# Performance work log

Hardware: AMD Instinct MI355X
Metric: run time of the kernel (lower is better)

Reference implementation:

```python
import jax, jax.numpy as jnp
from jax import lax
import numpy as np

# dims
V, D, T = 30000, 300, 24          # vocab, glove dim, seq len
H = 256                            # tweet_out_size == z_dim
NT, NU = 6000, 4000                # tweet nodes, user nodes
N = NT + NU
F, Z = 512, 256                    # user_feat_size, z_dim
E = 80000
B = 2000                           # batch_size (source tweets)
H1, H2, HEADS = 64, 100, 8
NEG = 0.2                          # GATConv default negative_slope


def setup_inputs() -> dict:
    k = jax.random.split(jax.random.key(0), 32)
    r = lambda i, shape, s=0.05: (s * jax.random.normal(k[i], shape)).astype(jnp.float32)
    return {
        "user_text": jax.random.randint(k[0], (B, T), 0, V),
        "user_feats": jax.random.normal(k[1], (NU, F), jnp.float32),
        "graph_node_features": jax.random.randint(k[2], (NT, T), 0, V),
        "graph_edge_index": jax.random.randint(k[3], (2, E), 0, N),
        "tweet_emb": r(4, (V, D), 0.1),
        "w_ih0": r(5, (3 * H, D)), "w_hh0": r(6, (3 * H, H)),
        "b_ih0": r(7, (3 * H,)), "b_hh0": r(8, (3 * H,)),
        "w_ih1": r(9, (3 * H, H)), "w_hh1": r(10, (3 * H, H)),
        "b_ih1": r(11, (3 * H,)), "b_hh1": r(12, (3 * H,)),
        "h0": r(13, (2, NT, H), 1.0),
        "w_mu": r(14, (Z, F)), "b_mu": r(15, (Z,)),
        "w_lv": r(16, (Z, F)), "b_lv": r(17, (Z,)),
        "w_dec": r(18, (F, Z)), "b_dec": r(19, (F,)),
        "vae_eps": r(20, (NU, Z), 1.0),
        "w1": r(21, (H, HEADS * H1)), "a_src1": r(22, (HEADS, H1)),
        "a_dst1": r(23, (HEADS, H1)), "b1": r(24, (HEADS * H1,)),
        "w2": r(25, (HEADS * H1, H2)), "a_src2": r(26, (1, H2)),
        "a_dst2": r(27, (1, H2)), "b2": r(28, (H2,)),
    }


def _gru_layer(x_seq, h0, w_ih, w_hh, b_ih, b_hh):
    # x_seq: [T, B, in]; torch nn.GRU gate math
    def step(h, x):
        gi = x @ w_ih.T + b_ih
        gh = h @ w_hh.T + b_hh
        i_r, i_z, i_n = jnp.split(gi, 3, axis=-1)
        h_r, h_z, h_n = jnp.split(gh, 3, axis=-1)
        r = jax.nn.sigmoid(i_r + h_r)
        z = jax.nn.sigmoid(i_z + h_z)
        n = jnp.tanh(i_n + r * h_n)
        hn = (1.0 - z) * n + z * h
        return hn, hn
    h_last, out = lax.scan(step, h0, x_seq)
    return out, h_last


def _gat(x, src, dst, w, a_src, a_dst, bias, heads, out_ch, concat):
    # PyG GATConv (eval mode, self-loops already appended)
    n = x.shape[0]
    xp = (x @ w).reshape(n, heads, out_ch)          # [N, H, C]
    as_n = (xp * a_src).sum(-1)                     # [N, H]
    ad_n = (xp * a_dst).sum(-1)
    e = jax.nn.leaky_relu(as_n[src] + ad_n[dst], NEG)          # [E, H]
    emax = jax.ops.segment_max(e, dst, num_segments=n)         # edge-softmax over dst
    ee = jnp.exp(e - emax[dst])
    denom = jax.ops.segment_sum(ee, dst, num_segments=n)
    alpha = ee / denom[dst]
    out = jax.ops.segment_sum(xp[src] * alpha[:, :, None], dst, num_segments=n)
    out = out.reshape(n, heads * out_ch) if concat else out.mean(axis=1)
    return out + bias


def reference(user_text, user_feats, graph_node_features, graph_edge_index,
              tweet_emb, w_ih0, w_hh0, b_ih0, b_hh0, w_ih1, w_hh1, b_ih1, b_hh1,
              h0, w_mu, b_mu, w_lv, b_lv, w_dec, b_dec, vae_eps,
              w1, a_src1, a_dst1, b1, w2, a_src2, a_dst2, b2):
    # --- VAE user embedding ---
    mu = user_feats @ w_mu.T + b_mu
    logvar = user_feats @ w_lv.T + b_lv
    z = mu + jnp.exp(0.5 * logvar) * vae_eps        # reparameterized latent
    rec = z @ w_dec.T + b_dec
    kl_loss = (-0.5 * (1.0 + logvar - mu**2 - jnp.exp(logvar)).sum(-1)).mean()
    rec_loss = ((rec - user_feats) ** 2).mean()
    # --- tweet encoder: embedding lookup + 2-layer GRU ---
    xe = tweet_emb[graph_node_features].transpose(1, 0, 2)     # [T, NT, D]
    out0, _ = _gru_layer(xe, h0[0], w_ih0, w_hh0, b_ih0, b_hh0)
    _, hn = _gru_layer(out0, h0[1], w_ih1, w_hh1, b_ih1, b_hh1)  # [NT, H]
    # --- assemble node features: source tweets, users, other tweets ---
    x_in = jnp.concatenate([hn[:B], z, hn[B:]], axis=0)        # [N, H]
    loops = jnp.arange(x_in.shape[0])
    src = jnp.concatenate([graph_edge_index[0], loops])
    dst = jnp.concatenate([graph_edge_index[1], loops])
    x1 = _gat(x_in, src, dst, w1, a_src1, a_dst1, b1, HEADS, H1, True)
    x2 = _gat(x1, src, dst, w2, a_src2, a_dst2, b2, 1, H2, False)
    return x2, kl_loss, rec_loss
```

## Files before the change

kernel.cpp:

```cpp
#include <hip/hip_runtime.h>

#define V_ 30000
#define D_ 300
#define DP_ 320
#define T_ 24
#define H_ 256
#define NT_ 6000
#define NU_ 4000
#define N_ 10000
#define F_ 512
#define Z_ 256
#define E_ 80000
#define B_ 2000
#define H1_ 64
#define H2_ 100
#define HEADS_ 8
#define E2_ (E_ + N_)

typedef __bf16 bf16_t;
typedef bf16_t bf16x8 __attribute__((ext_vector_type(8)));
typedef float  f32x4  __attribute__((ext_vector_type(4)));

__device__ __forceinline__ void gll16(const bf16_t* g, bf16_t* l)
{
    __builtin_amdgcn_global_load_lds(
        (const __attribute__((address_space(1))) void*)g,
        (__attribute__((address_space(3))) void*)l, 16, 0, 0);
}

struct GCfg {
    const bf16_t* A; const bf16_t* B; const float* bias;
    float* Cf; bf16_t* Cb; int M, N, K, ldc;
    const int* gtok; int t0;
};

template<bool OUTBF>
__global__ __launch_bounds__(256) void mfma_gemm(GCfg g0, GCfg g1)
{
    const GCfg g = blockIdx.z ? g1 : g0;
    __shared__ __align__(16) bf16_t SMEM[16384];
    const int tid  = (int)threadIdx.x;
    const int wave = tid >> 6, lane = tid & 63;
    const int quad = lane >> 4, l16 = lane & 15;
    const int mq = (wave & 1) * 64, nq = (wave >> 1) * 64;

    int bx = (int)blockIdx.x, by = (int)blockIdx.y;
    {
        int gx = (int)gridDim.x, total = gx * (int)gridDim.y;
        if ((total & 7) == 0) {
            int L = by * gx + bx;
            int F = (L & 7) * (total >> 3) + (L >> 3);
            bx = F % gx;
            by = F / gx;
        }
    }
    const int mbase = by * 128, nbase = bx * 128;
    const int M = g.M, N = g.N, K = g.K, ldc = g.ldc;

    const bf16_t* agp[2];
    const bf16_t* bgp[2];
#pragma unroll
    for (int j = 0; j < 2; j++) {
        int i = wave * 128 + j * 64 + lane;
        int c = i >> 7, row = i & 127;
        int r = mbase + row; if (r >= M) r = M - 1;
        int src = g.gtok ? g.gtok[(r % NT_) * T_ + g.t0 + (r / NT_)] : r;
        agp[j] = g.A + (size_t)src * K + c * 8;
        int rb = nbase + row; if (rb >= N) rb = N - 1;
        bgp[j] = g.B + (size_t)rb * K + c * 8;
    }

    f32x4 acc[4][4];
#pragma unroll
    for (int mi = 0; mi < 4; mi++)
#pragma unroll
        for (int ni = 0; ni < 4; ni++) acc[mi][ni] = (f32x4){0.f, 0.f, 0.f, 0.f};

    auto stage = [&](int b, int k0) {
        bf16_t* ab = SMEM + b * 4096 + wave * 1024;
        bf16_t* bb = SMEM + 8192 + b * 4096 + wave * 1024;
        gll16(agp[0] + k0, ab);
        gll16(agp[1] + k0, ab + 512);
        gll16(bgp[0] + k0, bb);
        gll16(bgp[1] + k0, bb + 512);
    };

    const int niter = K >> 5;
    stage(0, 0);
    for (int ks = 0; ks < niter; ks++) {
        __syncthreads();
        if (ks + 1 < niter) stage((ks + 1) & 1, (ks + 1) * 32);
        const bf16_t* Ab = SMEM + (ks & 1) * 4096;
        const bf16_t* Bb = SMEM + 8192 + (ks & 1) * 4096;
        bf16x8 afr[4], bfr[4];
#pragma unroll
        for (int mi = 0; mi < 4; mi++)
            afr[mi] = *(const bf16x8*)(Ab + (size_t)(quad * 128 + mq + mi * 16 + l16) * 8);
#pragma unroll
        for (int ni = 0; ni < 4; ni++)
            bfr[ni] = *(const bf16x8*)(Bb + (size_t)(quad * 128 + nq + ni * 16 + l16) * 8);
#pragma unroll
        for (int mi = 0; mi < 4; mi++)
#pragma unroll
            for (int ni = 0; ni < 4; ni++)
                acc[mi][ni] = __builtin_amdgcn_mfma_f32_16x16x32_bf16(
                    afr[mi], bfr[ni], acc[mi][ni], 0, 0, 0);
    }

    if (OUTBF) {
        __syncthreads();
#pragma unroll
        for (int ni = 0; ni < 4; ni++) {
            int colc = nq + ni * 16 + l16;
            float bv = g.bias ? g.bias[nbase + colc] : 0.f;
            int cc = colc >> 3, off = colc & 7;
#pragma unroll
            for (int mi = 0; mi < 4; mi++)
#pragma unroll
                for (int r = 0; r < 4; r++) {
                    int row = mq + mi * 16 + quad * 4 + r;
                    int sw = (row ^ (row >> 3)) & 7;
                    SMEM[row * 128 + ((cc ^ sw) << 3) + off] =
                        (bf16_t)(acc[mi][ni][r] + bv);
                }
        }
        __syncthreads();
        {
            int row = tid >> 1, seg = tid & 1;
            int sw = (row ^ (row >> 3)) & 7;
            int growr = mbase + row;
            if (growr < M) {
#pragma unroll
                for (int q = 0; q < 8; q++) {
                    int cc = seg * 8 + q;
                    bf16x8 v = *(const bf16x8*)(SMEM + row * 128 + ((cc ^ sw) << 3));
                    *(bf16x8*)(g.Cb + (size_t)growr * ldc + nbase + cc * 8) = v;
                }
            }
        }
    } else {
#pragma unroll
        for (int ni = 0; ni < 4; ni++) {
            int col = nbase + nq + ni * 16 + l16;
            if (col >= N) continue;
            float bv = g.bias ? g.bias[col] : 0.f;
#pragma unroll
            for (int mi = 0; mi < 4; mi++)
#pragma unroll
                for (int r = 0; r < 4; r++) {
                    int row = mbase + mq + mi * 16 + quad * 4 + r;
                    if (row >= M) continue;
                    g.Cf[(size_t)row * ldc + col] = acc[mi][ni][r] + bv;
                }
        }
    }
}

struct MegaLay {
    const bf16_t* vocGi;
    const int*    gnf;
    const bf16_t* whh0;
    const bf16_t* wih1;
    const bf16_t* whh1;
    const float *bhh0, *bih1, *bhh1;
    const bf16_t* h0in;
    const bf16_t* h1in;
    bf16_t*       xinout;
};

__device__ __forceinline__ float rcp_(float x)
{
    float r;
    asm("v_rcp_f32 %0, %1" : "=v"(r) : "v"(x));
    return r;
}
__device__ __forceinline__ float sigm_(float x)
{
    return rcp_(1.f + __expf(-x));
}
__device__ __forceinline__ float tanh_(float x)
{
    x = fminf(fmaxf(x, -15.f), 15.f);
    float t = __expf(2.f * x);
    return 1.f - 2.f * rcp_(t + 1.f);
}

#define HSW(Hb, row, byte) ((char*)(Hb) + ((((row) * 512) + (byte)) ^ (((row) & 7) << 4)))

__global__ __launch_bounds__(512, 1) void gru_mega(MegaLay L)
{
    __shared__ __align__(16) bf16_t H0L[8192];
    __shared__ __align__(16) bf16_t H1L[8192];
    __shared__ int TOK[768];
    const int tid  = (int)threadIdx.x;
    const int wv   = tid >> 6, lane = tid & 63;
    const int quad = lane >> 4, l16 = lane & 15;
    const int row0 = (int)blockIdx.x * 32;

    for (int i = tid; i < 768; i += 512) {
        int gi = row0 * T_ + i; if (gi >= NT_ * T_) gi = NT_ * T_ - 1;
        TOK[i] = L.gnf[gi];
    }
#pragma unroll
    for (int i = 0; i < 2; i++) {
        int idx  = i * 512 + tid;
        int rowl = idx >> 5, seg = idx & 31;
        int grow = row0 + rowl; if (grow >= NT_) grow = NT_ - 1;
        *(bf16x8*)HSW(H0L, rowl, seg * 16) =
            *(const bf16x8*)(L.h0in + (size_t)grow * H_ + seg * 8);
        *(bf16x8*)HSW(H1L, rowl, seg * 16) =
            *(const bf16x8*)(L.h1in + (size_t)grow * H_ + seg * 8);
    }

    float bh0[3][2], brz1[2][2], bni1[2], bnh1[2];
#pragma unroll
    for (int jj = 0; jj < 2; jj++) {
        int col = wv * 32 + jj * 16 + l16;
        bh0[0][jj] = L.bhh0[col];
        bh0[1][jj] = L.bhh0[256 + col];
        bh0[2][jj] = L.bhh0[512 + col];
        brz1[0][jj] = L.bih1[col] + L.bhh1[col];
        brz1[1][jj] = L.bih1[256 + col] + L.bhh1[256 + col];
        bni1[jj]    = L.bih1[512 + col];
        bnh1[jj]    = L.bhh1[512 + col];
    }

    auto run_gemm = [&](auto&& loadA, const bf16_t* W,
                        f32x4 (&arz)[2][2][2], f32x4 (&an)[2][2]) {
#pragma unroll 2
        for (int ks = 0; ks < 8; ks++) {
            bf16x8 bfr[3][2];
#pragma unroll
            for (int g = 0; g < 3; g++)
#pragma unroll
                for (int jj = 0; jj < 2; jj++)
                    bfr[g][jj] = *(const bf16x8*)(W +
                        (((size_t)(g * 16 + wv * 2 + jj) * 8 + ks) << 9) + lane * 8);
            bf16x8 afr[2];
            loadA(afr, ks);
#pragma unroll
            for (int m = 0; m < 2; m++)
#pragma unroll
                for (int jj = 0; jj < 2; jj++) {
                    arz[m][0][jj] = __builtin_amdgcn_mfma_f32_16x16x32_bf16(
                        afr[m], bfr[0][jj], arz[m][0][jj], 0, 0, 0);
                    arz[m][1][jj] = __builtin_amdgcn_mfma_f32_16x16x32_bf16(
                        afr[m], bfr[1][jj], arz[m][1][jj], 0, 0, 0);
                    an[m][jj] = __builtin_amdgcn_mfma_f32_16x16x32_bf16(
                        afr[m], bfr[2][jj], an[m][jj], 0, 0, 0);
                }
        }
    };

    __syncthreads();

    for (int t = 0; t < T_; t++) {
        f32x4 arz[2][2][2], an_i[2][2], an_h[2][2], gin[2][2];

#pragma unroll
        for (int m = 0; m < 2; m++)
#pragma unroll
            for (int r2 = 0; r2 < 4; r2++) {
                int rowl = m * 16 + quad * 4 + r2;
                const bf16_t* gp = L.vocGi +
                    (size_t)TOK[rowl * T_ + t] * (3 * H_);
#pragma unroll
                for (int jj = 0; jj < 2; jj++) {
                    int col = wv * 32 + jj * 16 + l16;
                    arz[m][0][jj][r2] = (float)gp[col];
                    arz[m][1][jj][r2] = (float)gp[256 + col];
                    gin[m][jj][r2]    = (float)gp[512 + col];
                }
            }
#pragma unroll
        for (int m = 0; m < 2; m++)
#pragma unroll
            for (int jj = 0; jj < 2; jj++)
                an_h[m][jj] = (f32x4){0.f, 0.f, 0.f, 0.f};

        run_gemm([&](bf16x8* afr, int ks) {
#pragma unroll
            for (int m = 0; m < 2; m++)
                afr[m] = *(const bf16x8*)HSW(H0L, m * 16 + l16,
                                             ks * 64 + quad * 16);
        }, L.whh0, arz, an_h);
        __syncthreads();

#pragma unroll
        for (int m = 0; m < 2; m++)
#pragma unroll
            for (int jj = 0; jj < 2; jj++) {
                int col = wv * 32 + jj * 16 + l16;
#pragma unroll
                for (int r = 0; r < 4; r++) {
                    int rowl = m * 16 + quad * 4 + r;
                    float hold = (float)*(const bf16_t*)HSW(H0L, rowl, col * 2);
                    float rg = sigm_(arz[m][0][jj][r] + bh0[0][jj]);
                    float zg = sigm_(arz[m][1][jj][r] + bh0[1][jj]);
                    float ng = tanh_(gin[m][jj][r] +
                                     rg * (an_h[m][jj][r] + bh0[2][jj]));
                    *(bf16_t*)HSW(H0L, rowl, col * 2) =
                        (bf16_t)((1.f - zg) * ng + zg * hold);
                }
            }
        __syncthreads();

#pragma unroll
        for (int m = 0; m < 2; m++)
#pragma unroll
            for (int jj = 0; jj < 2; jj++) {
                arz[m][0][jj] = (f32x4){0.f, 0.f, 0.f, 0.f};
                arz[m][1][jj] = (f32x4){0.f, 0.f, 0.f, 0.f};
                an_i[m][jj]   = (f32x4){0.f, 0.f, 0.f, 0.f};
                an_h[m][jj]   = (f32x4){0.f, 0.f, 0.f, 0.f};
            }
        run_gemm([&](bf16x8* afr, int ks) {
#pragma unroll
            for (int m = 0; m < 2; m++)
                afr[m] = *(const bf16x8*)HSW(H0L, m * 16 + l16,
                                             ks * 64 + quad * 16);
        }, L.wih1, arz, an_i);
        run_gemm([&](bf16x8* afr, int ks) {
#pragma unroll
            for (int m = 0; m < 2; m++)
                afr[m] = *(const bf16x8*)HSW(H1L, m * 16 + l16,
                                             ks * 64 + quad * 16);
        }, L.whh1, arz, an_h);
        __syncthreads();

#pragma unroll
        for (int m = 0; m < 2; m++)
#pragma unroll
            for (int jj = 0; jj < 2; jj++) {
                int col = wv * 32 + jj * 16 + l16;
#pragma unroll
                for (int r = 0; r < 4; r++) {
                    int rowl = m * 16 + quad * 4 + r;
                    float hold = (float)*(const bf16_t*)HSW(H1L, rowl, col * 2);
                    float rg = sigm_(arz[m][0][jj][r] + brz1[0][jj]);
                    float zg = sigm_(arz[m][1][jj][r] + brz1[1][jj]);
                    float ng = tanh_(an_i[m][jj][r] + bni1[jj] +
                                     rg * (an_h[m][jj][r] + bnh1[jj]));
                    *(bf16_t*)HSW(H1L, rowl, col * 2) =
                        (bf16_t)((1.f - zg) * ng + zg * hold);
                }
            }
    }

    __syncthreads();
#pragma unroll
    for (int i = 0; i < 2; i++) {
        int idx  = i * 512 + tid;
        int rowl = idx >> 5, seg = idx & 31;
        int grow = row0 + rowl;
        if (grow < NT_) {
            int dst = (grow < B_) ? grow : (grow + NU_);
            bf16x8 v = *(const bf16x8*)HSW(H1L, rowl, seg * 16);
            *(bf16x8*)(L.xinout + (size_t)dst * H_ + seg * 8) = v;
        }
    }
}

struct SegD { const float* src; bf16_t* dst; int rows, cin, cout, transp; };
struct PrepArgs { SegD seg[11]; long long base[12]; int nseg; long long total; };

__global__ void prep_kern(PrepArgs pa)
{
    long long stride = (long long)gridDim.x * blockDim.x;
    for (long long i = (long long)blockIdx.x * blockDim.x + threadIdx.x;
         i < pa.total; i += stride) {
        int k = 0;
        while (k + 1 < pa.nseg && i >= pa.base[k + 1]) k++;
        long long local = i - pa.base[k];
        SegD sg = pa.seg[k];
        float v;
        if (sg.transp == 2) {
            int nks  = sg.cout >> 5;
            int o    = (int)local;
            int e    = o & 7;
            int lane = (o >> 3) & 63;
            int rest = o >> 9;
            int ks   = rest % nks;
            int gcb  = rest / nks;
            int r    = (gcb >> 4) * 256 + (gcb & 15) * 16 + (lane & 15);
            int kk   = ks * 32 + (lane >> 4) * 8 + e;
            v = (kk < sg.cin) ? sg.src[(size_t)r * sg.cin + kk] : 0.f;
        } else {
            int r = (int)(local / sg.cout);
            int c = (int)(local - (long long)r * sg.cout);
            if (sg.transp) v = sg.src[(size_t)c * sg.rows + r];
            else           v = (c < sg.cin) ? sg.src[(size_t)r * sg.cin + c] : 0.f;
        }
        sg.dst[local] = (bf16_t)v;
    }
}

__global__ void init_all(const float* __restrict__ h0in, bf16_t* __restrict__ h0b,
                         bf16_t* __restrict__ h1b,
                         int* __restrict__ deg, int* __restrict__ dcnt,
                         float* __restrict__ loss2, float* __restrict__ b_ml,
                         const float* __restrict__ b_mu, const float* __restrict__ b_lv)
{
    int i = blockIdx.x * blockDim.x + threadIdx.x;
    if (i < NT_ * H_) {
        h0b[i] = (bf16_t)h0in[i];
        h1b[i] = (bf16_t)h0in[NT_ * H_ + i];
    }
    if (i < N_) { deg[i] = 0; dcnt[i] = 0; }
    if (i < 2 * Z_) b_ml[i] = (i < Z_) ? b_mu[i] : b_lv[i - Z_];
    if (i < 2) loss2[i] = 0.f;
}

__device__ __forceinline__ void edge_sd(const int* __restrict__ ei, int e, int& s, int& d)
{
    if (e < E_) { s = ei[e]; d = ei[E_ + e]; }
    else        { s = d = e - E_; }
}

__global__ void csr_hist(const int* __restrict__ ei, int* __restrict__ deg)
{
    int e = blockIdx.x * blockDim.x + threadIdx.x;
    if (e >= E2_) return;
    int s, d; edge_sd(ei, e, s, d);
    atomicAdd(deg + d, 1);
}

__global__ void csr_scan(const int* __restrict__ deg, int* __restrict__ rowptr)
{
    __shared__ int buf[256];
    __shared__ int carry;
    int tid = (int)threadIdx.x;
    if (tid == 0) { carry = 0; rowptr[0] = 0; }
    __syncthreads();
    for (int c0 = 0; c0 < N_; c0 += 256) {
        int i = c0 + tid;
        buf[tid] = (i < N_) ? deg[i] : 0;
        __syncthreads();
        for (int off = 1; off < 256; off <<= 1) {
            int t = (tid >= off) ? buf[tid - off] : 0;
            __syncthreads();
            buf[tid] += t;
            __syncthreads();
        }
        if (i < N_) rowptr[i + 1] = carry + buf[tid];
        __syncthreads();
        if (tid == 255) carry += buf[255];
        __syncthreads();
    }
}

__global__ void csr_scatter(const int* __restrict__ ei, const int* __restrict__ rowptr,
                            int* __restrict__ dcnt, int* __restrict__ csrc)
{
    int e = blockIdx.x * blockDim.x + threadIdx.x;
    if (e >= E2_) return;
    int s, d; edge_sd(ei, e, s, d);
    int pos = rowptr[d] + atomicAdd(dcnt + d, 1);
    csrc[pos] = s;
}

__global__ __launch_bounds__(256) void vae_z_kl(
    const float* __restrict__ ml, const float* __restrict__ eps,
    bf16_t* __restrict__ z_out, float* __restrict__ kl_out)
{
    float t = 0.f;
    int stride = (int)gridDim.x * 256;
    for (int idx = blockIdx.x * 256 + threadIdx.x; idx < NU_ * Z_; idx += stride) {
        int row = idx >> 8, c = idx & 255;
        float m = ml[(size_t)row * 512 + c];
        float l = ml[(size_t)row * 512 + 256 + c];
        float el = expf(l);
        z_out[idx] = (bf16_t)(m + expf(0.5f * l) * eps[idx]);
        t += -0.5f * (1.f + l - m * m - el);
    }
    __shared__ float red[256];
    red[threadIdx.x] = t;
    __syncthreads();
    for (int s = 128; s > 0; s >>= 1) {
        if ((int)threadIdx.x < s) red[threadIdx.x] += red[threadIdx.x + s];
        __syncthreads();
    }
    if (threadIdx.x == 0) atomicAdd(kl_out, red[0] * (1.f / NU_));
}

__global__ __launch_bounds__(256) void rec_loss_kern(
    const float* __restrict__ rec, const float* __restrict__ uf,
    float* __restrict__ loss_out)
{
    float t = 0.f;
    int stride = (int)gridDim.x * 256;
    for (int idx = blockIdx.x * 256 + threadIdx.x; idx < NU_ * F_; idx += stride) {
        float d = rec[idx] - uf[idx];
        t += d * d;
    }
    __shared__ float red[256];
    red[threadIdx.x] = t;
    __syncthreads();
    for (int s = 128; s > 0; s >>= 1) {
        if ((int)threadIdx.x < s) red[threadIdx.x] += red[threadIdx.x + s];
        __syncthreads();
    }
    if (threadIdx.x == 0) atomicAdd(loss_out, red[0] * (1.f / (NU_ * F_)));
}

__global__ __launch_bounds__(256) void gat_agg1(
    const int* __restrict__ rowptr, const int* __restrict__ csrc,
    const bf16_t* __restrict__ xp, const float* __restrict__ a_src,
    const float* __restrict__ a_dst, const float* __restrict__ bias,
    bf16_t* __restrict__ x1out)
{
    int d = blockIdx.x;
    int tid = (int)threadIdx.x;
    int w = tid >> 6, lane = tid & 63;
    int h0 = w, h1 = w + 4;
    float as0 = a_src[h0 * 64 + lane], as1 = a_src[h1 * 64 + lane];
    float adv0 = a_dst[h0 * 64 + lane], adv1 = a_dst[h1 * 64 + lane];
    int beg = rowptr[d], end = rowptr[d + 1];

    float t0 = (float)xp[(size_t)d * 512 + tid] * adv0;
    float t1 = (float)xp[(size_t)d * 512 + 256 + tid] * adv1;
#pragma unroll
    for (int mk = 1; mk < 64; mk <<= 1) {
        t0 += __shfl_xor(t0, mk);
        t1 += __shfl_xor(t1, mk);
    }
    float ad0 = t0, ad1 = t1;

    float m0 = -1e30f, m1 = -1e30f;
    float den0 = 0.f, den1 = 0.f, acc0 = 0.f, acc1 = 0.f;
    for (int e = beg; e < end; e++) {
        int s = csrc[e];
        float x0 = (float)xp[(size_t)s * 512 + tid];
        float x1 = (float)xp[(size_t)s * 512 + 256 + tid];
        float s0 = x0 * as0, s1 = x1 * as1;
#pragma unroll
        for (int mk = 1; mk < 64; mk <<= 1) {
            s0 += __shfl_xor(s0, mk);
            s1 += __shfl_xor(s1, mk);
        }
        float l0 = s0 + ad0; l0 = (l0 > 0.f) ? l0 : 0.2f * l0;
        float l1 = s1 + ad1; l1 = (l1 > 0.f) ? l1 : 0.2f * l1;
        float M0 = fmaxf(m0, l0), sc0 = __expf(m0 - M0), p0 = __expf(l0 - M0);
        den0 = den0 * sc0 + p0; acc0 = acc0 * sc0 + p0 * x0; m0 = M0;
        float M1 = fmaxf(m1, l1), sc1 = __expf(m1 - M1), p1 = __expf(l1 - M1);
        den1 = den1 * sc1 + p1; acc1 = acc1 * sc1 + p1 * x1; m1 = M1;
    }
    x1out[(size_t)d * 512 + tid]       = (bf16_t)(bias[tid] + acc0 / den0);
    x1out[(size_t)d * 512 + 256 + tid] = (bf16_t)(bias[256 + tid] + acc1 / den1);
}

__global__ __launch_bounds__(256) void gat_agg2(
    const int* __restrict__ rowptr, const int* __restrict__ csrc,
    const float* __restrict__ xp, const float* __restrict__ a_src,
    const float* __restrict__ a_dst, const float* __restrict__ bias,
    float* __restrict__ outp)
{
    int d = blockIdx.x * 4 + ((int)threadIdx.x >> 6);
    if (d >= N_) return;
    int lane = (int)threadIdx.x & 63;
    int hi = (lane < H2_ - 64);
    float a0 = a_src[lane], a1 = hi ? a_src[64 + lane] : 0.f;
    float b0 = a_dst[lane], b1 = hi ? a_dst[64 + lane] : 0.f;
    int beg = rowptr[d], end = rowptr[d + 1];

    float xd0 = xp[(size_t)d * H2_ + lane];
    float xd1 = hi ? xp[(size_t)d * H2_ + 64 + lane] : 0.f;
    float t = xd0 * b0 + xd1 * b1;
#pragma unroll
    for (int mk = 1; mk < 64; mk <<= 1) t += __shfl_xor(t, mk);
    float adnd = t;

    float mx = -1e30f, den = 0.f, acc0 = 0.f, acc1 = 0.f;
    for (int e = beg; e < end; e++) {
        int s = csrc[e];
        float x0 = xp[(size_t)s * H2_ + lane];
        float x1 = hi ? xp[(size_t)s * H2_ + 64 + lane] : 0.f;
        float sd = x0 * a0 + x1 * a1;
#pragma unroll
        for (int mk = 1; mk < 64; mk <<= 1) sd += __shfl_xor(sd, mk);
        float l = sd + adnd;
        l = (l > 0.f) ? l : 0.2f * l;
        float M = fmaxf(mx, l), sc = __expf(mx - M), p = __expf(l - M);
        den = den * sc + p;
        acc0 = acc0 * sc + p * x0;
        acc1 = acc1 * sc + p * x1;
        mx = M;
    }
    outp[(size_t)d * H2_ + lane] = bias[lane] + acc0 / den;
    if (hi)
        outp[(size_t)d * H2_ + 64 + lane] = bias[64 + lane] + acc1 / den;
}

extern "C" void kernel_launch(void* const* d_in, const int* in_sizes, int n_in,
                              void* d_out, int out_size, void* d_ws, size_t ws_size,
                              hipStream_t stream)
{
    const float* user_feats = (const float*)d_in[1];
    const int*   gnf        = (const int*)d_in[2];
    const int*   ei         = (const int*)d_in[3];
    const float* temb       = (const float*)d_in[4];
    const float* w_ih0      = (const float*)d_in[5];
    const float* w_hh0      = (const float*)d_in[6];
    const float* b_ih0      = (const float*)d_in[7];
    const float* b_hh0      = (const float*)d_in[8];
    const float* w_ih1      = (const float*)d_in[9];
    const float* w_hh1      = (const float*)d_in[10];
    const float* b_ih1      = (const float*)d_in[11];
    const float* b_hh1      = (const float*)d_in[12];
    const float* h0in       = (const float*)d_in[13];
    const float* w_mu       = (const float*)d_in[14];
    const float* b_mu       = (const float*)d_in[15];
    const float* w_lv       = (const float*)d_in[16];
    const float* b_lv       = (const float*)d_in[17];
    const float* w_dec      = (const float*)d_in[18];
    const float* b_dec      = (const float*)d_in[19];
    const float* veps       = (const float*)d_in[20];
    const float* w1         = (const float*)d_in[21];
    const float* a_src1     = (const float*)d_in[22];
    const float* a_dst1     = (const float*)d_in[23];
    const float* b1         = (const float*)d_in[24];
    const float* w2         = (const float*)d_in[25];
    const float* a_src2     = (const float*)d_in[26];
    const float* a_dst2     = (const float*)d_in[27];
    const float* b2         = (const float*)d_in[28];
    float* out = (float*)d_out;

    char* wsb = (char*)d_ws;
    bf16_t* temb_bf = (bf16_t*)(wsb + 0);
    bf16_t* vocGi   = (bf16_t*)(wsb + 19200000);
    float*  mlbuf   = (float*)(wsb + 66000000);
    float*  recb    = (float*)(wsb + 75000000);
    bf16_t* xp1b    = (bf16_t*)(wsb + 0);
    bf16_t* x1b     = (bf16_t*)(wsb + 20480000);
    float*  xp2     = (float*)(wsb + 30720000);
    bf16_t* wih0_bf = (bf16_t*)(wsb + 92928000);
    bf16_t* whh0_bf = (bf16_t*)(wsb + 93419520);
    bf16_t* wih1_bf = (bf16_t*)(wsb + 93812736);
    bf16_t* whh1_bf = (bf16_t*)(wsb + 94205952);
    bf16_t* wml_bf  = (bf16_t*)(wsb + 94599168);
    bf16_t* wdec_bf = (bf16_t*)(wsb + 95123456);
    bf16_t* w1t_bf  = (bf16_t*)(wsb + 95385600);
    bf16_t* w2t_bf  = (bf16_t*)(wsb + 95648000);
    float*  b_ml    = (float*)(wsb + 95750400);
    bf16_t* ufeats_bf = (bf16_t*)(wsb + 95752448);
    bf16_t* h0b_init = (bf16_t*)(wsb + 124424448);
    bf16_t* h1init  = (bf16_t*)(wsb + 127496448);
    bf16_t* xin_bf  = (bf16_t*)(wsb + 136712448);
    int*    deg     = (int*)(wsb + 141832448);
    int*    dcnt    = (int*)(wsb + 141872448);
    int*    rowptr  = (int*)(wsb + 141912448);
    int*    csrc    = (int*)(wsb + 141952512);

    const int TB = 256;
    auto blocks = [](int n) { return (n + 255) / 256; };

    auto mkcfg = [](const bf16_t* A, const bf16_t* B, const float* bias,
                    float* Cf, bf16_t* Cb, int M, int N, int K, int ldc,
                    const int* gtok, int t0) {
        GCfg g; g.A = A; g.B = B; g.bias = bias; g.Cf = Cf; g.Cb = Cb;
        g.M = M; g.N = N; g.K = K; g.ldc = ldc; g.gtok = gtok; g.t0 = t0;
        return g;
    };
    auto launch_bf = [&](GCfg g0) {
        dim3 grid((g0.N + 127) / 128, (g0.M + 127) / 128, 1);
        hipLaunchKernelGGL((mfma_gemm<true>), grid, dim3(TB), 0, stream, g0, g0);
    };
    auto launch_f32 = [&](GCfg g0) {
        dim3 grid((g0.N + 127) / 128, (g0.M + 127) / 128, 1);
        hipLaunchKernelGGL((mfma_gemm<false>), grid, dim3(TB), 0, stream, g0, g0);
    };

    PrepArgs pa;
    auto seg = [&](int k, const float* s, bf16_t* dst, int rows, int cin, int cout, int tr) {
        pa.seg[k] = SegD{s, dst, rows, cin, cout, tr};
    };
    seg(0, temb, temb_bf, V_, D_, DP_, 0);
    seg(1, w_ih0, wih0_bf, 3 * H_, D_, DP_, 0);
    seg(2, w_hh0, whh0_bf, 3 * H_, H_, H_, 2);
    seg(3, w_ih1, wih1_bf, 3 * H_, H_, H_, 2);
    seg(4, w_hh1, whh1_bf, 3 * H_, H_, H_, 2);
    seg(5, w_mu, wml_bf, Z_, F_, F_, 0);
    seg(6, w_lv, wml_bf + (size_t)Z_ * F_, Z_, F_, F_, 0);
    seg(7, w_dec, wdec_bf, F_, Z_, Z_, 0);
    seg(8, user_feats, ufeats_bf, NU_, F_, F_, 0);
    seg(9, w1, w1t_bf, HEADS_ * H1_, 0, H_, 1);
    seg(10, w2, w2t_bf, H2_, 0, HEADS_ * H1_, 1);
    pa.nseg = 11;
    long long acc = 0;
    for (int k = 0; k < 11; k++) {
        pa.base[k] = acc;
        acc += (long long)pa.seg[k].rows * pa.seg[k].cout;
    }
    pa.base[11] = acc;
    pa.total = acc;
    hipLaunchKernelGGL(prep_kern, dim3(6144), dim3(TB), 0, stream, pa);

    hipLaunchKernelGGL(init_all, dim3(blocks(NT_ * H_)), dim3(TB), 0, stream,
                       h0in, h0b_init, h1init,
                       deg, dcnt, out + N_ * H2_, b_ml, b_mu, b_lv);

    hipLaunchKernelGGL(csr_hist, dim3(blocks(E2_)), dim3(TB), 0, stream, ei, deg);
    hipLaunchKernelGGL(csr_scan, dim3(1), dim3(TB), 0, stream, deg, rowptr);
    hipLaunchKernelGGL(csr_scatter, dim3(blocks(E2_)), dim3(TB), 0, stream,
                       ei, rowptr, dcnt, csrc);

    launch_bf(mkcfg(temb_bf, wih0_bf, b_ih0, nullptr, vocGi,
                    V_, 3 * H_, DP_, 3 * H_, nullptr, 0));

    launch_f32(mkcfg(ufeats_bf, wml_bf, b_ml, mlbuf, nullptr,
                     NU_, 2 * Z_, F_, 2 * Z_, nullptr, 0));
    bf16_t* z_bf = xin_bf + (size_t)B_ * H_;
    hipLaunchKernelGGL(vae_z_kl, dim3(256), dim3(TB), 0, stream,
                       mlbuf, veps, z_bf, out + N_ * H2_);
    launch_f32(mkcfg(z_bf, wdec_bf, b_dec, recb, nullptr,
                     NU_, F_, Z_, F_, nullptr, 0));
    hipLaunchKernelGGL(rec_loss_kern, dim3(256), dim3(TB), 0, stream,
                       recb, user_feats, out + N_ * H2_ + 1);

    {
        MegaLay ML;
        ML.vocGi = vocGi; ML.gnf = gnf;
        ML.whh0 = whh0_bf; ML.wih1 = wih1_bf; ML.whh1 = whh1_bf;
        ML.bhh0 = b_hh0; ML.bih1 = b_ih1; ML.bhh1 = b_hh1;
        ML.h0in = h0b_init; ML.h1in = h1init; ML.xinout = xin_bf;
        hipLaunchKernelGGL(gru_mega, dim3((NT_ + 31) / 32), dim3(512), 0, stream, ML);
    }

    launch_bf(mkcfg(xin_bf, w1t_bf, nullptr, nullptr, xp1b,
                    N_, HEADS_ * H1_, H_, HEADS_ * H1_, nullptr, 0));
    hipLaunchKernelGGL(gat_agg1, dim3(N_), dim3(TB), 0, stream,
                       rowptr, csrc, xp1b, a_src1, a_dst1, b1, x1b);

    launch_f32(mkcfg(x1b, w2t_bf, nullptr, xp2, nullptr,
                     N_, H2_, HEADS_ * H1_, H2_, nullptr, 0));
    hipLaunchKernelGGL(gat_agg2, dim3((N_ + 3) / 4), dim3(TB), 0, stream,
                       rowptr, csrc, xp2, a_src2, a_dst2, b2, out);

    (void)in_sizes; (void)n_in; (void)out_size; (void)ws_size;
}
```

Before: 794.2 us.

## Software-pipeline GRU weight loads with double-buffered fragments and register-resident first slices

Replaces the generic per-step GEMM loop with explicitly double-buffered B-fragment loads, so global weight fetches for k-slice ks+2 are issued while MFMAs run on earlier slices. The first k-slices of whh0 and wih1 are kept in registers across all timesteps, and the second slice is prefetched before the barrier and gate math. This hides load latency at the cost of higher register pressure. It also removes the tanh input clamp and rewrites the GRU blend to use one fewer multiply; without the clamp, exp may overflow to inf, though the rcp-based form still saturates correctly.

```diff
diff --git a/kernel.cpp b/kernel.cpp
--- a/kernel.cpp
+++ b/kernel.cpp
@@ -180,7 +180,6 @@
 }
 __device__ __forceinline__ float tanh_(float x)
 {
-    x = fminf(fmaxf(x, -15.f), 15.f);
     float t = __expf(2.f * x);
     return 1.f - 2.f * rcp_(t + 1.f);
 }
@@ -225,38 +224,88 @@
         bnh1[jj]    = L.bhh1[512 + col];
     }
 
-    auto run_gemm = [&](auto&& loadA, const bf16_t* W,
-                        f32x4 (&arz)[2][2][2], f32x4 (&an)[2][2]) {
-#pragma unroll 2
-        for (int ks = 0; ks < 8; ks++) {
-            bf16x8 bfr[3][2];
-#pragma unroll
-            for (int g = 0; g < 3; g++)
-#pragma unroll
-                for (int jj = 0; jj < 2; jj++)
-                    bfr[g][jj] = *(const bf16x8*)(W +
-                        (((size_t)(g * 16 + wv * 2 + jj) * 8 + ks) << 9) + lane * 8);
-            bf16x8 afr[2];
-            loadA(afr, ks);
-#pragma unroll
-            for (int m = 0; m < 2; m++)
-#pragma unroll
-                for (int jj = 0; jj < 2; jj++) {
-                    arz[m][0][jj] = __builtin_amdgcn_mfma_f32_16x16x32_bf16(
-                        afr[m], bfr[0][jj], arz[m][0][jj], 0, 0, 0);
-                    arz[m][1][jj] = __builtin_amdgcn_mfma_f32_16x16x32_bf16(
-                        afr[m], bfr[1][jj], arz[m][1][jj], 0, 0, 0);
-                    an[m][jj] = __builtin_amdgcn_mfma_f32_16x16x32_bf16(
-                        afr[m], bfr[2][jj], an[m][jj], 0, 0, 0);
-                }
-        }
-    };
+    auto loadB = [&](bf16x8 (&b)[3][2], const bf16_t* W, int ks) {
+#pragma unroll
+        for (int g = 0; g < 3; g++)
+#pragma unroll
+            for (int jj = 0; jj < 2; jj++)
+                b[g][jj] = *(const bf16x8*)(W +
+                    (((size_t)(g * 16 + wv * 2 + jj) * 8 + ks) << 9) + lane * 8);
+    };
+
+    f32x4 arz[2][2][2], an_i[2][2], an_h[2][2], gin[2][2];
+    auto mfma12 = [&](const bf16x8 (&b)[3][2], const bf16x8 (&afr)[2],
+                      f32x4 (&an)[2][2]) {
+#pragma unroll
+        for (int m = 0; m < 2; m++)
+#pragma unroll
+            for (int jj = 0; jj < 2; jj++) {
+                arz[m][0][jj] = __builtin_amdgcn_mfma_f32_16x16x32_bf16(
+                    afr[m], b[0][jj], arz[m][0][jj], 0, 0, 0);
+                arz[m][1][jj] = __builtin_amdgcn_mfma_f32_16x16x32_bf16(
+                    afr[m], b[1][jj], arz[m][1][jj], 0, 0, 0);
+                an[m][jj] = __builtin_amdgcn_mfma_f32_16x16x32_bf16(
+                    afr[m], b[2][jj], an[m][jj], 0, 0, 0);
+            }
+    };
+    auto ldA0 = [&](bf16x8 (&afr)[2], int ks) {
+#pragma unroll
+        for (int m = 0; m < 2; m++)
+            afr[m] = *(const bf16x8*)HSW(H0L, m * 16 + l16, ks * 64 + quad * 16);
+    };
+    auto ldA1 = [&](bf16x8 (&afr)[2], int ks) {
+#pragma unroll
+        for (int m = 0; m < 2; m++)
+            afr[m] = *(const bf16x8*)HSW(H1L, m * 16 + l16, ks * 64 + quad * 16);
+    };
+
+    auto run_p = [&](auto&& loadA, const bf16_t* W,
+                     const bf16x8 (&k0)[3][2], const bf16x8 (&kpre)[3][2],
+                     f32x4 (&an)[2][2]) {
+        bf16x8 s0[3][2], s1[3][2], afr[2];
+        loadB(s0, W, 2);
+        loadA(afr, 0); mfma12(k0, afr, an);
+        loadB(s1, W, 3);
+        loadA(afr, 1); mfma12(kpre, afr, an);
+        loadA(afr, 2); mfma12(s0, afr, an);
+        loadB(s0, W, 4);
+        loadA(afr, 3); mfma12(s1, afr, an);
+        loadB(s1, W, 5);
+        loadA(afr, 4); mfma12(s0, afr, an);
+        loadB(s0, W, 6);
+        loadA(afr, 5); mfma12(s1, afr, an);
+        loadB(s1, W, 7);
+        loadA(afr, 6); mfma12(s0, afr, an);
+        loadA(afr, 7); mfma12(s1, afr, an);
+    };
+    auto run_r = [&](auto&& loadA, const bf16_t* W, f32x4 (&an)[2][2]) {
+        bf16x8 s0[3][2], s1[3][2], afr[2];
+        loadB(s0, W, 0);
+        loadB(s1, W, 1);
+        loadA(afr, 0); mfma12(s0, afr, an);
+        loadB(s0, W, 2);
+        loadA(afr, 1); mfma12(s1, afr, an);
+        loadB(s1, W, 3);
+        loadA(afr, 2); mfma12(s0, afr, an);
+        loadB(s0, W, 4);
+        loadA(afr, 3); mfma12(s1, afr, an);
+        loadB(s1, W, 5);
+        loadA(afr, 4); mfma12(s0, afr, an);
+        loadB(s0, W, 6);
+        loadA(afr, 5); mfma12(s1, afr, an);
+        loadB(s1, W, 7);
+        loadA(afr, 6); mfma12(s0, afr, an);
+        loadA(afr, 7); mfma12(s1, afr, an);
+    };
+
+    bf16x8 K00[3][2], K01[3][2], kpre[3][2];
+    loadB(K00, L.whh0, 0);
+    loadB(K01, L.wih1, 0);
+    loadB(kpre, L.whh0, 1);
 
     __syncthreads();
 
     for (int t = 0; t < T_; t++) {
-        f32x4 arz[2][2][2], an_i[2][2], an_h[2][2], gin[2][2];
-
 #pragma unroll
         for (int m = 0; m < 2; m++)
 #pragma unroll
@@ -278,12 +327,8 @@
             for (int jj = 0; jj < 2; jj++)
                 an_h[m][jj] = (f32x4){0.f, 0.f, 0.f, 0.f};
 
-        run_gemm([&](bf16x8* afr, int ks) {
-#pragma unroll
-            for (int m = 0; m < 2; m++)
-                afr[m] = *(const bf16x8*)HSW(H0L, m * 16 + l16,
-                                             ks * 64 + quad * 16);
-        }, L.whh0, arz, an_h);
+        run_p(ldA0, L.whh0, K00, kpre, an_h);
+        loadB(kpre, L.wih1, 1);
         __syncthreads();
 
 #pragma unroll
@@ -300,7 +345,7 @@
                     float ng = tanh_(gin[m][jj][r] +
                                      rg * (an_h[m][jj][r] + bh0[2][jj]));
                     *(bf16_t*)HSW(H0L, rowl, col * 2) =
-                        (bf16_t)((1.f - zg) * ng + zg * hold);
+                        (bf16_t)(ng + zg * (hold - ng));
                 }
             }
         __syncthreads();
@@ -314,18 +359,9 @@
                 an_i[m][jj]   = (f32x4){0.f, 0.f, 0.f, 0.f};
                 an_h[m][jj]   = (f32x4){0.f, 0.f, 0.f, 0.f};
             }
-        run_gemm([&](bf16x8* afr, int ks) {
-#pragma unroll
-            for (int m = 0; m < 2; m++)
-                afr[m] = *(const bf16x8*)HSW(H0L, m * 16 + l16,
-                                             ks * 64 + quad * 16);
-        }, L.wih1, arz, an_i);
-        run_gemm([&](bf16x8* afr, int ks) {
-#pragma unroll
-            for (int m = 0; m < 2; m++)
-                afr[m] = *(const bf16x8*)HSW(H1L, m * 16 + l16,
-                                             ks * 64 + quad * 16);
-        }, L.whh1, arz, an_h);
+        run_p(ldA0, L.wih1, K01, kpre, an_i);
+        run_r(ldA1, L.whh1, an_h);
+        loadB(kpre, L.whh0, 1);
         __syncthreads();
 
 #pragma unroll
@@ -342,7 +378,7 @@
                     float ng = tanh_(an_i[m][jj][r] + bni1[jj] +
                                      rg * (an_h[m][jj][r] + bnh1[jj]));
                     *(bf16_t*)HSW(H1L, rowl, col * 2) =
-                        (bf16_t)((1.f - zg) * ng + zg * hold);
+                        (bf16_t)(ng + zg * (hold - ng));
                 }
             }
     }
```

Result: slower. 1.411 ms (+77.6%).
